# Performance work log

Measured on AMD Instinct MI355X. Metric: run time of the kernel, lower is better.

## Reference

```python
import jax, jax.numpy as jnp
import numpy as np

N = 100000     # total points
PBS = 500      # point_batch_size (hard-coded in module)
K = 100        # num_neighbors
KP = 15        # num_kernel_points
EPS = 1e-5


def _bn(x, g, b, axes):
    # torch BatchNorm in training mode: batch stats, biased variance
    m = jnp.mean(x, axis=axes, keepdims=True)
    v = jnp.var(x, axis=axes, keepdims=True)
    return (x - m) / jnp.sqrt(v + EPS) * g + b


def setup_inputs() -> dict:
    key = jax.random.key(0)
    ks = jax.random.split(key, 16)
    rn = lambda k, sh, s=1.0: jax.random.normal(k, sh, jnp.float32) * s
    return {
        "pts": rn(ks[0], (N, 3)),
        "normal": rn(ks[1], (N, 3)),
        "kp_points": rn(ks[2], (KP, 3)),
        "kp_weights": rn(ks[3], (KP, 3, 128), 0.3),
        "kp_sigma": jnp.float32(1.0),
        "conv1_w": rn(ks[4], (1024, 128), 128 ** -0.5),
        "conv1_b": rn(ks[5], (1024,), 0.02),
        "bn1_g": jnp.ones((1024,), jnp.float32),
        "bn1_b": jnp.zeros((1024,), jnp.float32),
        "fc1_w": rn(ks[6], (512, 1024), 1024 ** -0.5),
        "fc1_b": rn(ks[7], (512,), 0.02),
        "bn4_g": jnp.ones((512,), jnp.float32),
        "bn4_b": jnp.zeros((512,), jnp.float32),
        "fc2_w": rn(ks[8], (256, 512), 512 ** -0.5),
        "fc2_b": rn(ks[9], (256,), 0.02),
        "bn5_g": jnp.ones((256,), jnp.float32),
        "bn5_b": jnp.zeros((256,), jnp.float32),
        "fc3_w": rn(ks[10], (3, 256), 256 ** -0.5),
        "fc3_b": rn(ks[11], (3,), 0.02),
        "index": jax.random.randint(ks[12], (PBS,), 0, N, jnp.int32),
    }


def reference(pts, normal, kp_points, kp_weights, kp_sigma,
              conv1_w, conv1_b, bn1_g, bn1_b,
              fc1_w, fc1_b, bn4_g, bn4_b,
              fc2_w, fc2_b, bn5_g, bn5_b,
              fc3_w, fc3_b, index):
    sel = pts[index]                                               # [B,3]
    # L-inf pairwise distance and kNN (topk of -dist, as in the torch code)
    dist = jnp.max(jnp.abs(sel[:, None, :] - pts[None, :, :]), axis=-1)  # [B,N]
    _, nbr = jax.lax.top_k(-dist, K)                               # [B,K]
    rel = pts[nbr] - sel[:, None, :]                               # [B,K,3]

    # KPConv: gaussian weights vs kernel points, per-kernel-point linear map
    d2 = jnp.sum((rel[:, :, None, :] - kp_points[None, None]) ** 2, axis=-1)  # [B,K,KP]
    w = jnp.exp(-0.5 * d2 / (kp_sigma ** 2))
    wf = rel[:, :, None, :] * w[..., None]                         # [B,K,KP,3]
    h = jax.nn.relu(jnp.einsum('bnkc,kco->bno', wf, kp_weights))   # [B,K,128]

    # 1x1 conv 128->1024, relu then BN over (batch, points) per channel
    h = jnp.einsum('bnc,oc->bno', h, conv1_w) + conv1_b            # [B,K,1024]
    h = _bn(jax.nn.relu(h), bn1_g, bn1_b, (0, 1))
    feat = jnp.max(h, axis=1)                                      # [B,1024]

    feat = _bn(jax.nn.relu(feat @ fc1_w.T + fc1_b), bn4_g, bn4_b, (0,))
    feat = _bn(jax.nn.relu(feat @ fc2_w.T + fc2_b), bn5_g, bn5_b, (0,))
    feat = feat @ fc3_w.T + fc3_b                                  # [B,3]
    return feat, normal[index]
```

## Files before the change

kernel.cpp:

```cpp
#include <hip/hip_runtime.h>
#include <hip/hip_fp16.h>

#define NPTS 100000
#define NB 500
#define KNN 100
#define KPN 15
#define C1 128
#define C2 1024
#define C3 512
#define C4 256

#define G 64
#define NCELLS (G * G * G)
#define GB 5.0f
#define GINVH ((float)G / (2.f * GB))
#define CAND_CAP 2048

typedef _Float16 half8 __attribute__((ext_vector_type(8)));
typedef float f32x4 __attribute__((ext_vector_type(4)));

__global__ __launch_bounds__(256) void prep_kernel(
    const float* __restrict__ pts, const float* __restrict__ normal,
    const int* __restrict__ index, const float* __restrict__ w1,
    const float* __restrict__ kpw, float* __restrict__ sel,
    float* __restrict__ out2, __half* __restrict__ wh,
    __half* __restrict__ kpwT_hi, __half* __restrict__ kpwT_lo) {
  int i = blockIdx.x * 256 + threadIdx.x;
  if (i < NB) {
    int ix = index[i];
    sel[i * 3 + 0] = pts[3 * ix + 0];
    sel[i * 3 + 1] = pts[3 * ix + 1];
    sel[i * 3 + 2] = pts[3 * ix + 2];
    out2[i * 3 + 0] = normal[3 * ix + 0];
    out2[i * 3 + 1] = normal[3 * ix + 1];
    out2[i * 3 + 2] = normal[3 * ix + 2];
  }
  if (i < C2 * C1) wh[i] = __float2half(w1[i]);
  if (i < 128 * 64) {
    int o = i >> 6, j = i & 63;
    float v = (j < 45) ? kpw[j * 128 + o] : 0.f;
    __half hi = __float2half_rn(v);
    kpwT_hi[i] = hi;
    kpwT_lo[i] = __float2half_rn(v - __half2float(hi));
  }
}

__device__ __forceinline__ int cell_coord(float x) {
  int c = (int)floorf((x + GB) * GINVH);
  return min(max(c, 0), G - 1);
}
__device__ __forceinline__ int cell_of(float x, float y, float z) {
  return (cell_coord(x) << 12) | (cell_coord(y) << 6) | cell_coord(z);
}

__global__ __launch_bounds__(256) void grid_hist_kernel(
    const float* __restrict__ pts, unsigned* __restrict__ cnt) {
  int i = blockIdx.x * 256 + threadIdx.x;
  if (i >= NPTS) return;
  atomicAdd(&cnt[cell_of(pts[3 * i], pts[3 * i + 1], pts[3 * i + 2])], 1u);
}

__global__ __launch_bounds__(256) void grid_scan1_kernel(
    const unsigned* __restrict__ cnt, unsigned* __restrict__ cursor,
    unsigned* __restrict__ chunktot) {
  const int tid = threadIdx.x;
  int base = blockIdx.x * 1024 + tid * 4;
  unsigned c0 = cnt[base], c1 = cnt[base + 1], c2 = cnt[base + 2],
           c3 = cnt[base + 3];
  unsigned tot = c0 + c1 + c2 + c3;
  __shared__ unsigned sb[256];
  sb[tid] = tot;
  __syncthreads();
  for (int off = 1; off < 256; off <<= 1) {
    unsigned add = (tid >= off) ? sb[tid - off] : 0u;
    __syncthreads();
    sb[tid] += add;
    __syncthreads();
  }
  unsigned excl = sb[tid] - tot;
  cursor[base] = excl;
  cursor[base + 1] = excl + c0;
  cursor[base + 2] = excl + c0 + c1;
  cursor[base + 3] = excl + c0 + c1 + c2;
  if (tid == 255) chunktot[blockIdx.x] = sb[255];
}

__global__ __launch_bounds__(256) void grid_scan2_kernel(
    const unsigned* __restrict__ chunktot, unsigned* __restrict__ chunkoff) {
  const int tid = threadIdx.x;
  unsigned v = chunktot[tid];
  __shared__ unsigned sb[256];
  sb[tid] = v;
  __syncthreads();
  for (int off = 1; off < 256; off <<= 1) {
    unsigned add = (tid >= off) ? sb[tid - off] : 0u;
    __syncthreads();
    sb[tid] += add;
    __syncthreads();
  }
  chunkoff[tid] = sb[tid] - v;
}

__global__ __launch_bounds__(256) void grid_scan3_kernel(
    unsigned* __restrict__ cursor, const unsigned* __restrict__ chunkoff) {
  unsigned off = chunkoff[blockIdx.x];
  int base = blockIdx.x * 1024 + threadIdx.x * 4;
#pragma unroll
  for (int j = 0; j < 4; ++j) cursor[base + j] += off;
}

__global__ __launch_bounds__(256) void grid_scatter_kernel(
    const float* __restrict__ pts, unsigned* __restrict__ cursor,
    float4* __restrict__ sorted) {
  int i = blockIdx.x * 256 + threadIdx.x;
  if (i >= NPTS) return;
  float x = pts[3 * i], y = pts[3 * i + 1], z = pts[3 * i + 2];
  unsigned pos = atomicAdd(&cursor[cell_of(x, y, z)], 1u);
  sorted[pos] = make_float4(x, y, z, __int_as_float(i));
}

__device__ __forceinline__ unsigned linf_bits(float px, float py, float pz,
                                              float sx, float sy, float sz) {
  float dx = fabsf(px - sx), dy = fabsf(py - sy), dz = fabsf(pz - sz);
  return __float_as_uint(fmaxf(fmaxf(dx, dy), dz));
}

__global__ __launch_bounds__(256) void knn_kernel(
    const float4* __restrict__ sorted, const unsigned* __restrict__ cnt,
    const unsigned* __restrict__ cursor,
    const float* __restrict__ sel, int* __restrict__ nbr) {
  const int b = blockIdx.x;
  const int tid = threadIdx.x;
  __shared__ unsigned cbits[CAND_CAP];
  __shared__ int cidx[CAND_CAP];
  __shared__ unsigned hist[4096];
  __shared__ unsigned scanbuf[256];
  __shared__ int s_total, s_m, s_mc, s_chunk;
  __shared__ unsigned s_excl, s_bub;

  const float qx = sel[b * 3 + 0], qy = sel[b * 3 + 1], qz = sel[b * 3 + 2];
  const int qcx = cell_coord(qx), qcy = cell_coord(qy), qcz = cell_coord(qz);

  int s = 0;
  int xlo, xhi, ylo, yhi, zlo, zhi;
  for (;;) {
    if (tid == 0) s_total = 0;
    __syncthreads();
    xlo = max(qcx - s, 0); xhi = min(qcx + s, G - 1);
    ylo = max(qcy - s, 0); yhi = min(qcy + s, G - 1);
    zlo = max(qcz - s, 0); zhi = min(qcz + s, G - 1);
    int nx = xhi - xlo + 1, ny = yhi - ylo + 1, nz = zhi - zlo + 1;
    int ncell = nx * ny * nz;
    unsigned local = 0;
    for (int ci = tid; ci < ncell; ci += 256) {
      int cz = ci % nz;
      int r = ci / nz;
      int cy = r % ny;
      int cx = r / ny;
      local += cnt[((xlo + cx) << 12) | ((ylo + cy) << 6) | (zlo + cz)];
    }
#pragma unroll
    for (int off = 32; off; off >>= 1) local += __shfl_down(local, off);
    if ((tid & 63) == 0) atomicAdd(&s_total, (int)local);
    __syncthreads();
    if (s_total >= KNN || (xlo == 0 && ylo == 0 && zlo == 0 && xhi == G - 1 &&
                           yhi == G - 1 && zhi == G - 1))
      break;
    ++s;
    __syncthreads();
  }

  if (tid == 0) s_m = 0;
  __syncthreads();
  {
    int nx = xhi - xlo + 1, ny = yhi - ylo + 1, nz = zhi - zlo + 1;
    int ncell = nx * ny * nz;
    for (int ci = tid; ci < ncell; ci += 256) {
      int cz = ci % nz;
      int r = ci / nz;
      int cy = r % ny;
      int cx = r / ny;
      int cell = ((xlo + cx) << 12) | ((ylo + cy) << 6) | (zlo + cz);
      unsigned end = cursor[cell];
      unsigned beg = end - cnt[cell];
      for (unsigned p = beg; p < end; ++p) {
        float4 f = sorted[p];
        unsigned bits = linf_bits(f.x, f.y, f.z, qx, qy, qz);
        int e = atomicAdd(&s_m, 1);
        if (e < CAND_CAP) {
          cbits[e] = bits;
          cidx[e] = __float_as_int(f.w);
        }
      }
    }
  }
  __syncthreads();
  int m = s_m < CAND_CAP ? s_m : CAND_CAP;

  for (int j = tid; j < 4096; j += 256) hist[j] = 0;
  __syncthreads();
  for (int e = tid; e < m; e += 256) atomicAdd(&hist[cbits[e] >> 19], 1u);
  __syncthreads();
  unsigned csum = 0;
  {
    int c0 = tid * 16;
#pragma unroll
    for (int j = 0; j < 16; ++j) csum += hist[c0 + j];
  }
  scanbuf[tid] = csum;
  __syncthreads();
  for (int off = 1; off < 256; off <<= 1) {
    unsigned add = (tid >= off) ? scanbuf[tid - off] : 0u;
    __syncthreads();
    scanbuf[tid] += add;
    __syncthreads();
  }
  {
    unsigned incl = scanbuf[tid], excl = incl - csum;
    if (excl < KNN && KNN <= incl) {
      s_chunk = tid;
      s_excl = excl;
    }
  }
  __syncthreads();
  if (tid == 0) {
    unsigned cum = s_excl;
    int bin = s_chunk * 16;
    while (cum + hist[bin] < KNN) {
      cum += hist[bin];
      ++bin;
    }
    s_bub = (unsigned)(bin + 1) << 19;
  }
  __syncthreads();

  const unsigned bub = s_bub;
  const float dub = __uint_as_float(bub);
  if (tid == 0) s_mc = 0;
  __syncthreads();
  {
    int xlo2 = min(max((int)floorf((qx - dub + GB) * GINVH), 0), G - 1);
    int xhi2 = min(max((int)floorf((qx + dub + GB) * GINVH), 0), G - 1);
    int ylo2 = min(max((int)floorf((qy - dub + GB) * GINVH), 0), G - 1);
    int yhi2 = min(max((int)floorf((qy + dub + GB) * GINVH), 0), G - 1);
    int zlo2 = min(max((int)floorf((qz - dub + GB) * GINVH), 0), G - 1);
    int zhi2 = min(max((int)floorf((qz + dub + GB) * GINVH), 0), G - 1);
    int nx = xhi2 - xlo2 + 1, ny = yhi2 - ylo2 + 1, nz = zhi2 - zlo2 + 1;
    int ncell = nx * ny * nz;
    for (int ci = tid; ci < ncell; ci += 256) {
      int cz = ci % nz;
      int r = ci / nz;
      int cy = r % ny;
      int cx = r / ny;
      int cell = ((xlo2 + cx) << 12) | ((ylo2 + cy) << 6) | (zlo2 + cz);
      unsigned end = cursor[cell];
      unsigned beg = end - cnt[cell];
      for (unsigned p = beg; p < end; ++p) {
        float4 f = sorted[p];
        unsigned bits = linf_bits(f.x, f.y, f.z, qx, qy, qz);
        if (bits < bub) {
          int e = atomicAdd(&s_mc, 1);
          if (e < CAND_CAP) {
            cbits[e] = bits;
            cidx[e] = __float_as_int(f.w);
          }
        }
      }
    }
  }
  __syncthreads();
  int mc = s_mc < CAND_CAP ? s_mc : CAND_CAP;

  for (int c = tid; c < mc; c += 256) {
    unsigned bc = cbits[c];
    int ic = cidx[c];
    int rank = 0;
    for (int j = 0; j < mc; ++j) {
      unsigned bj = cbits[j];
      rank += (bj < bc || (bj == bc && cidx[j] < ic)) ? 1 : 0;
    }
    if (rank < KNN) nbr[b * KNN + rank] = ic;
  }
}

__global__ __launch_bounds__(256) void kpconv_mfma_kernel(
    const float* __restrict__ pts, const float* __restrict__ sel,
    const int* __restrict__ nbr, const float* __restrict__ kp_points,
    const __half* __restrict__ kpwT_hi, const __half* __restrict__ kpwT_lo,
    const float* __restrict__ kp_sigma, __half* __restrict__ h) {
  const int b = blockIdx.x;
  const int tid = threadIdx.x;
  const int wave = tid >> 6, lane = tid & 63;
  const int lr = lane & 15, quad = lane >> 4;
  __shared__ __half As_hi[112 * 72];
  __shared__ __half As_lo[112 * 72];
  __shared__ __half Bs_hi[128 * 72];
  __shared__ __half Bs_lo[128 * 72];
  __shared__ float rel[100][4];
  __shared__ float kpp[48];

  for (int i = tid; i < 128 * 8; i += 256) {
    int row = i >> 3, seg = i & 7;
    *(float4*)&Bs_hi[row * 72 + seg * 8] =
        *(const float4*)&kpwT_hi[row * 64 + seg * 8];
    *(float4*)&Bs_lo[row * 72 + seg * 8] =
        *(const float4*)&kpwT_lo[row * 64 + seg * 8];
  }
  {
    float4 z = make_float4(0.f, 0.f, 0.f, 0.f);
    for (int i = tid; i < 112 * 8; i += 256) {
      int row = i >> 3, seg = i & 7;
      *(float4*)&As_hi[row * 72 + seg * 8] = z;
      *(float4*)&As_lo[row * 72 + seg * 8] = z;
    }
  }
  if (tid < 45) kpp[tid] = kp_points[tid];
  if (tid < 100) {
    int idx = nbr[b * KNN + tid];
    rel[tid][0] = pts[3 * idx + 0] - sel[b * 3 + 0];
    rel[tid][1] = pts[3 * idx + 1] - sel[b * 3 + 1];
    rel[tid][2] = pts[3 * idx + 2] - sel[b * 3 + 2];
  }
  __syncthreads();

  const float sg = kp_sigma[0];
  const float inv2s2 = -0.5f / (sg * sg);
  for (int i = tid; i < 100 * KPN; i += 256) {
    int k = i / KPN, p = i - k * KPN;
    float rx = rel[k][0] - kpp[p * 3 + 0];
    float ry = rel[k][1] - kpp[p * 3 + 1];
    float rz = rel[k][2] - kpp[p * 3 + 2];
    float w = expf(inv2s2 * (rx * rx + ry * ry + rz * rz));
#pragma unroll
    for (int c = 0; c < 3; ++c) {
      float a = rel[k][c] * w;
      __half hi = __float2half_rn(a);
      As_hi[k * 72 + p * 3 + c] = hi;
      As_lo[k * 72 + p * 3 + c] = __float2half_rn(a - __half2float(hi));
    }
  }
  __syncthreads();

  f32x4 acc[2][7];
#pragma unroll
  for (int t = 0; t < 2; ++t)
#pragma unroll
    for (int m = 0; m < 7; ++m) acc[t][m] = (f32x4)(0.f);

#pragma unroll
  for (int s = 0; s < 2; ++s) {
    half8 bhi[2], blo[2];
#pragma unroll
    for (int t = 0; t < 2; ++t) {
      int boff = ((wave * 2 + t) * 16 + lr) * 72 + s * 32 + quad * 8;
      bhi[t] = *(const half8*)&Bs_hi[boff];
      blo[t] = *(const half8*)&Bs_lo[boff];
    }
#pragma unroll
    for (int m = 0; m < 7; ++m) {
      int aoff = (m * 16 + lr) * 72 + s * 32 + quad * 8;
      half8 ahi = *(const half8*)&As_hi[aoff];
      half8 alo = *(const half8*)&As_lo[aoff];
#pragma unroll
      for (int t = 0; t < 2; ++t) {
        acc[t][m] = __builtin_amdgcn_mfma_f32_16x16x32_f16(ahi, bhi[t],
                                                           acc[t][m], 0, 0, 0);
        acc[t][m] = __builtin_amdgcn_mfma_f32_16x16x32_f16(ahi, blo[t],
                                                           acc[t][m], 0, 0, 0);
        acc[t][m] = __builtin_amdgcn_mfma_f32_16x16x32_f16(alo, bhi[t],
                                                           acc[t][m], 0, 0, 0);
      }
    }
  }

#pragma unroll
  for (int t = 0; t < 2; ++t) {
    int col = (wave * 2 + t) * 16 + lr;
#pragma unroll
    for (int m = 0; m < 7; ++m)
#pragma unroll
      for (int r = 0; r < 4; ++r) {
        int row = m * 16 + quad * 4 + r;
        if (row < 100)
          h[(b * KNN + row) * 128 + col] =
              __float2half_rn(fmaxf(acc[t][m][r], 0.f));
      }
  }
}

__global__ __launch_bounds__(256) void conv1_mfma_kernel(
    const __half* __restrict__ h16, const __half* __restrict__ wh,
    const float* __restrict__ bias, float* __restrict__ featmax,
    float* __restrict__ featmin, float* __restrict__ bnsum,
    float* __restrict__ bnsq) {
  const int b = blockIdx.y;
  const int n0 = blockIdx.x * 128;
  const int tid = threadIdx.x;
  const int wave = tid >> 6, lane = tid & 63;
  const int lr = lane & 15, quad = lane >> 4;
  __shared__ __half Hs[112 * 136];
  __shared__ __half Ws[128 * 136];

  for (int i = tid; i < 112 * 16; i += 256) {
    int row = i >> 4, seg = i & 15;
    float4 v = make_float4(0.f, 0.f, 0.f, 0.f);
    if (row < 100) v = *(const float4*)&h16[(b * 100 + row) * 128 + seg * 8];
    *(float4*)&Hs[row * 136 + seg * 8] = v;
  }
  for (int i = tid; i < 128 * 16; i += 256) {
    int row = i >> 4, seg = i & 15;
    *(float4*)&Ws[row * 136 + seg * 8] =
        *(const float4*)&wh[(n0 + row) * 128 + seg * 8];
  }
  __syncthreads();

  f32x4 acc[2][7];
#pragma unroll
  for (int t = 0; t < 2; ++t)
#pragma unroll
    for (int m = 0; m < 7; ++m) acc[t][m] = (f32x4)(0.f);

#pragma unroll
  for (int s = 0; s < 4; ++s) {
    half8 bfrag[2];
#pragma unroll
    for (int t = 0; t < 2; ++t)
      bfrag[t] =
          *(const half8*)&Ws[((wave * 2 + t) * 16 + lr) * 136 + s * 32 + quad * 8];
#pragma unroll
    for (int m = 0; m < 7; ++m) {
      half8 afrag = *(const half8*)&Hs[(m * 16 + lr) * 136 + s * 32 + quad * 8];
      acc[0][m] =
          __builtin_amdgcn_mfma_f32_16x16x32_f16(afrag, bfrag[0], acc[0][m], 0, 0, 0);
      acc[1][m] =
          __builtin_amdgcn_mfma_f32_16x16x32_f16(afrag, bfrag[1], acc[1][m], 0, 0, 0);
    }
  }

#pragma unroll
  for (int t = 0; t < 2; ++t) {
    int col = n0 + (wave * 2 + t) * 16 + lr;
    float bv = bias[col];
    float pmax = -1e30f, pmin = 1e30f, psum = 0.f, psq = 0.f;
#pragma unroll
    for (int m = 0; m < 7; ++m)
#pragma unroll
      for (int r = 0; r < 4; ++r) {
        int row = m * 16 + quad * 4 + r;
        if (row < 100) {
          float y = fmaxf(acc[t][m][r] + bv, 0.f);
          pmax = fmaxf(pmax, y);
          pmin = fminf(pmin, y);
          psum += y;
          psq += y * y;
        }
      }
    pmax = fmaxf(pmax, __shfl_xor(pmax, 16));
    pmax = fmaxf(pmax, __shfl_xor(pmax, 32));
    pmin = fminf(pmin, __shfl_xor(pmin, 16));
    pmin = fminf(pmin, __shfl_xor(pmin, 32));
    psum += __shfl_xor(psum, 16);
    psum += __shfl_xor(psum, 32);
    psq += __shfl_xor(psq, 16);
    psq += __shfl_xor(psq, 32);
    if (quad == 0) {
      featmax[b * C2 + col] = pmax;
      featmin[b * C2 + col] = pmin;
      atomicAdd(&bnsum[col], psum);
      atomicAdd(&bnsq[col], psq);
    }
  }
}

__global__ __launch_bounds__(256) void bn1max_kernel(
    const float* __restrict__ featmax, const float* __restrict__ featmin,
    const float* __restrict__ bnsum, const float* __restrict__ bnsq,
    const float* __restrict__ g, const float* __restrict__ bb,
    float* __restrict__ feat1) {
  int idx = blockIdx.x * 256 + threadIdx.x;
  if (idx >= NB * C2) return;
  int o = idx & (C2 - 1);
  const float invn = 1.f / (float)(NB * KNN);
  float m = bnsum[o] * invn;
  float v = bnsq[o] * invn - m * m;
  float a = g[o] / sqrtf(v + 1e-5f);
  float x = (a >= 0.f) ? featmax[idx] : featmin[idx];
  feat1[idx] = (x - m) * a + bb[o];
}

template <int KDIM>
__global__ __launch_bounds__(256) void fc_relu_stats_kernel(
    const float* __restrict__ x,
    const float* __restrict__ w,
    const float* __restrict__ bias, float* __restrict__ yraw,
    float* __restrict__ s, float* __restrict__ sq, int ncols) {
  const int r0 = blockIdx.x * 4;
  const int n0 = blockIdx.y * 64;
  const int tid = threadIdx.x;
  const int col = tid >> 2;
  const int row = tid & 3;
  __shared__ float xs[4][1028];
  __shared__ float ws[64][132];
  for (int f = tid; f < KDIM; f += 256) {
    int rr = f / (KDIM / 4), kq = (f % (KDIM / 4)) * 4;
    *(float4*)&xs[rr][kq] = *(const float4*)&x[(r0 + rr) * KDIM + kq];
  }
  float acc = 0.f;
  for (int kc = 0; kc < KDIM; kc += 128) {
    __syncthreads();
#pragma unroll
    for (int i = 0; i < 8; ++i) {
      int f = tid + i * 256;
      int cr = f >> 5, kq = (f & 31) * 4;
      *(float4*)&ws[cr][kq] = *(const float4*)&w[(n0 + cr) * KDIM + kc + kq];
    }
    __syncthreads();
    for (int kk = 0; kk < 128; kk += 4) {
      float4 xv = *(float4*)&xs[row][kc + kk];
      float4 wv = *(float4*)&ws[col][kk];
      acc += xv.x * wv.x + xv.y * wv.y + xv.z * wv.z + xv.w * wv.w;
    }
  }
  float y = fmaxf(acc + bias[n0 + col], 0.f);
  yraw[(r0 + row) * ncols + n0 + col] = y;
  float ys = y, y2 = y * y;
  ys += __shfl_xor(ys, 1); y2 += __shfl_xor(y2, 1);
  ys += __shfl_xor(ys, 2); y2 += __shfl_xor(y2, 2);
  if (row == 0) {
    atomicAdd(&s[n0 + col], ys);
    atomicAdd(&sq[n0 + col], y2);
  }
}

__global__ __launch_bounds__(256) void bn_finalize_kernel(
    const float* __restrict__ yraw, const float* __restrict__ s,
    const float* __restrict__ sq, const float* __restrict__ g,
    const float* __restrict__ bb, float* __restrict__ out, int ncols) {
  int idx = blockIdx.x * 256 + threadIdx.x;
  if (idx >= NB * ncols) return;
  int o = idx & (ncols - 1);
  float m = s[o] * (1.f / (float)NB);
  float v = sq[o] * (1.f / (float)NB) - m * m;
  float a = g[o] / sqrtf(v + 1e-5f);
  out[idx] = (yraw[idx] - m) * a + bb[o];
}

__global__ __launch_bounds__(256) void fc3_kernel(
    const float* __restrict__ feat, const float* __restrict__ w,
    const float* __restrict__ bias, float* __restrict__ out) {
  int idx = blockIdx.x * 256 + threadIdx.x;
  if (idx >= NB * 3) return;
  int b = idx / 3, o = idx % 3;
  float acc = 0.f;
  for (int k = 0; k < C4; ++k) acc += feat[b * C4 + k] * w[o * C4 + k];
  out[idx] = acc + bias[o];
}

extern "C" void kernel_launch(void* const* d_in, const int* in_sizes, int n_in,
                              void* d_out, int out_size, void* d_ws,
                              size_t ws_size, hipStream_t stream) {
  const float* pts = (const float*)d_in[0];
  const float* normal = (const float*)d_in[1];
  const float* kp_points = (const float*)d_in[2];
  const float* kp_weights = (const float*)d_in[3];
  const float* kp_sigma = (const float*)d_in[4];
  const float* conv1_w = (const float*)d_in[5];
  const float* conv1_b = (const float*)d_in[6];
  const float* bn1_g = (const float*)d_in[7];
  const float* bn1_b = (const float*)d_in[8];
  const float* fc1_w = (const float*)d_in[9];
  const float* fc1_b = (const float*)d_in[10];
  const float* bn4_g = (const float*)d_in[11];
  const float* bn4_b = (const float*)d_in[12];
  const float* fc2_w = (const float*)d_in[13];
  const float* fc2_b = (const float*)d_in[14];
  const float* bn5_g = (const float*)d_in[15];
  const float* bn5_b = (const float*)d_in[16];
  const float* fc3_w = (const float*)d_in[17];
  const float* fc3_b = (const float*)d_in[18];
  const int* index = (const int*)d_in[19];
  float* out = (float*)d_out;

  char* p = (char*)d_ws;
  auto carve = [&](size_t bytes) {
    void* r = (void*)p;
    p += (bytes + 255) & ~(size_t)255;
    return r;
  };
  float* sel = (float*)carve(NB * 3 * 4);
  int* nbr = (int*)carve(NB * KNN * 4);
  __half* h = (__half*)carve((size_t)NB * KNN * C1 * 2);
  __half* wh = (__half*)carve((size_t)C2 * C1 * 2);
  __half* kpwT_hi = (__half*)carve((size_t)128 * 64 * 2);
  __half* kpwT_lo = (__half*)carve((size_t)128 * 64 * 2);
  float* featmax = (float*)carve(NB * C2 * 4);
  float* featmin = (float*)carve(NB * C2 * 4);
  float* feat1 = (float*)carve(NB * C2 * 4);
  float* f2raw = (float*)carve(NB * C3 * 4);
  float* feat2 = (float*)carve(NB * C3 * 4);
  float* f3raw = (float*)carve(NB * C4 * 4);
  float* feat3 = (float*)carve(NB * C4 * 4);
  float* stats = (float*)carve((2 * C2 + 2 * C3 + 2 * C4) * 4);
  float* bnsum = stats;
  float* bnsq = stats + C2;
  float* s4 = stats + 2 * C2;
  float* sq4 = s4 + C3;
  float* s5 = sq4 + C3;
  float* sq5 = s5 + C4;

  {
    char* gp = (char*)h;
    auto gcarve = [&](size_t bytes) {
      void* r = (void*)gp;
      gp += (bytes + 255) & ~(size_t)255;
      return r;
    };
    unsigned* cellcnt = (unsigned*)gcarve((size_t)NCELLS * 4);
    unsigned* cellcur = (unsigned*)gcarve((size_t)NCELLS * 4);
    unsigned* chunktot = (unsigned*)gcarve(256 * 4);
    unsigned* chunkoff = (unsigned*)gcarve(256 * 4);
    float4* sortedpts = (float4*)gcarve((size_t)NPTS * 16);

    hipMemsetAsync(stats, 0, (2 * C2 + 2 * C3 + 2 * C4) * 4, stream);
    hipMemsetAsync(cellcnt, 0, (size_t)NCELLS * 4, stream);

    prep_kernel<<<(C2 * C1 + 255) / 256, 256, 0, stream>>>(
        pts, normal, index, conv1_w, kp_weights, sel, out + NB * 3, wh,
        kpwT_hi, kpwT_lo);
    grid_hist_kernel<<<(NPTS + 255) / 256, 256, 0, stream>>>(pts, cellcnt);
    grid_scan1_kernel<<<256, 256, 0, stream>>>(cellcnt, cellcur, chunktot);
    grid_scan2_kernel<<<1, 256, 0, stream>>>(chunktot, chunkoff);
    grid_scan3_kernel<<<256, 256, 0, stream>>>(cellcur, chunkoff);
    grid_scatter_kernel<<<(NPTS + 255) / 256, 256, 0, stream>>>(pts, cellcur,
                                                                sortedpts);
    knn_kernel<<<NB, 256, 0, stream>>>(sortedpts, cellcnt, cellcur, sel, nbr);
  }

  kpconv_mfma_kernel<<<NB, 256, 0, stream>>>(pts, sel, nbr, kp_points, kpwT_hi,
                                             kpwT_lo, kp_sigma, h);
  conv1_mfma_kernel<<<dim3(8, NB), 256, 0, stream>>>(h, wh, conv1_b, featmax,
                                                     featmin, bnsum, bnsq);
  bn1max_kernel<<<(NB * C2 + 255) / 256, 256, 0, stream>>>(
      featmax, featmin, bnsum, bnsq, bn1_g, bn1_b, feat1);
  fc_relu_stats_kernel<C2><<<dim3(125, C3 / 64), 256, 0, stream>>>(
      feat1, fc1_w, fc1_b, f2raw, s4, sq4, C3);
  bn_finalize_kernel<<<(NB * C3 + 255) / 256, 256, 0, stream>>>(
      f2raw, s4, sq4, bn4_g, bn4_b, feat2, C3);
  fc_relu_stats_kernel<C3><<<dim3(125, C4 / 64), 256, 0, stream>>>(
      feat2, fc2_w, fc2_b, f3raw, s5, sq5, C4);
  bn_finalize_kernel<<<(NB * C4 + 255) / 256, 256, 0, stream>>>(
      f3raw, s5, sq5, bn5_g, bn5_b, feat3, C4);
  fc3_kernel<<<(NB * 3 + 255) / 256, 256, 0, stream>>>(feat3, fc3_w, fc3_b,
                                                       out);
}
```

Before: 298.1 us.

## Fuse KPConv and conv1 into one kernel keeping features in shared memory

Merges the KPConv MFMA kernel and the 128->1024 conv1 MFMA kernel into one per-batch-point kernel. The KPConv output is written to shared memory instead of a global fp16 buffer, and the block then loops over eight 128-column chunks of the conv1 weights, reusing the same shared tile. This removes the global write and read of the intermediate features and one launch. In exchange the grid shrinks from 4000 blocks to 500, each doing serial work. The larger shared memory footprint (~71KB) may also cut occupancy.

```diff
diff --git a/kernel.cpp b/kernel.cpp
--- a/kernel.cpp
+++ b/kernel.cpp
@@ -283,21 +283,28 @@
   }
 }
 
-__global__ __launch_bounds__(256) void kpconv_mfma_kernel(
+__global__ __launch_bounds__(256) void kpconv_conv1_kernel(
     const float* __restrict__ pts, const float* __restrict__ sel,
     const int* __restrict__ nbr, const float* __restrict__ kp_points,
     const __half* __restrict__ kpwT_hi, const __half* __restrict__ kpwT_lo,
-    const float* __restrict__ kp_sigma, __half* __restrict__ h) {
+    const float* __restrict__ kp_sigma, const __half* __restrict__ wh,
+    const float* __restrict__ bias, float* __restrict__ featmax,
+    float* __restrict__ featmin, float* __restrict__ bnsum,
+    float* __restrict__ bnsq) {
   const int b = blockIdx.x;
   const int tid = threadIdx.x;
   const int wave = tid >> 6, lane = tid & 63;
   const int lr = lane & 15, quad = lane >> 4;
-  __shared__ __half As_hi[112 * 72];
-  __shared__ __half As_lo[112 * 72];
-  __shared__ __half Bs_hi[128 * 72];
-  __shared__ __half Bs_lo[128 * 72];
-  __shared__ float rel[100][4];
-  __shared__ float kpp[48];
+
+  __shared__ __align__(16) char smem[71168];
+  __half* As_hi = (__half*)smem;
+  __half* As_lo = As_hi + 112 * 72;
+  __half* Bs_hi = As_lo + 112 * 72;
+  __half* Bs_lo = Bs_hi + 128 * 72;
+  float* rel = (float*)(Bs_lo + 128 * 72);
+  float* kpp = rel + 100 * 4;
+  __half* Hs = (__half*)smem;
+  __half* Ws = Hs + 112 * 136;
 
   for (int i = tid; i < 128 * 8; i += 256) {
     int row = i >> 3, seg = i & 7;
@@ -317,9 +324,9 @@
   if (tid < 45) kpp[tid] = kp_points[tid];
   if (tid < 100) {
     int idx = nbr[b * KNN + tid];
-    rel[tid][0] = pts[3 * idx + 0] - sel[b * 3 + 0];
-    rel[tid][1] = pts[3 * idx + 1] - sel[b * 3 + 1];
-    rel[tid][2] = pts[3 * idx + 2] - sel[b * 3 + 2];
+    rel[tid * 4 + 0] = pts[3 * idx + 0] - sel[b * 3 + 0];
+    rel[tid * 4 + 1] = pts[3 * idx + 1] - sel[b * 3 + 1];
+    rel[tid * 4 + 2] = pts[3 * idx + 2] - sel[b * 3 + 2];
   }
   __syncthreads();
 
@@ -327,13 +334,13 @@
   const float inv2s2 = -0.5f / (sg * sg);
   for (int i = tid; i < 100 * KPN; i += 256) {
     int k = i / KPN, p = i - k * KPN;
-    float rx = rel[k][0] - kpp[p * 3 + 0];
-    float ry = rel[k][1] - kpp[p * 3 + 1];
-    float rz = rel[k][2] - kpp[p * 3 + 2];
+    float rx = rel[k * 4 + 0] - kpp[p * 3 + 0];
+    float ry = rel[k * 4 + 1] - kpp[p * 3 + 1];
+    float rz = rel[k * 4 + 2] - kpp[p * 3 + 2];
     float w = expf(inv2s2 * (rx * rx + ry * ry + rz * rz));
 #pragma unroll
     for (int c = 0; c < 3; ++c) {
-      float a = rel[k][c] * w;
+      float a = rel[k * 4 + c] * w;
       __half hi = __float2half_rn(a);
       As_hi[k * 72 + p * 3 + c] = hi;
       As_lo[k * 72 + p * 3 + c] = __float2half_rn(a - __half2float(hi));
@@ -372,6 +379,7 @@
       }
     }
   }
+  __syncthreads();
 
 #pragma unroll
   for (int t = 0; t < 2; ++t) {
@@ -381,93 +389,75 @@
 #pragma unroll
       for (int r = 0; r < 4; ++r) {
         int row = m * 16 + quad * 4 + r;
-        if (row < 100)
-          h[(b * KNN + row) * 128 + col] =
-              __float2half_rn(fmaxf(acc[t][m][r], 0.f));
+        Hs[row * 136 + col] = __float2half_rn(fmaxf(acc[t][m][r], 0.f));
       }
   }
-}
-
-__global__ __launch_bounds__(256) void conv1_mfma_kernel(
-    const __half* __restrict__ h16, const __half* __restrict__ wh,
-    const float* __restrict__ bias, float* __restrict__ featmax,
-    float* __restrict__ featmin, float* __restrict__ bnsum,
-    float* __restrict__ bnsq) {
-  const int b = blockIdx.y;
-  const int n0 = blockIdx.x * 128;
-  const int tid = threadIdx.x;
-  const int wave = tid >> 6, lane = tid & 63;
-  const int lr = lane & 15, quad = lane >> 4;
-  __shared__ __half Hs[112 * 136];
-  __shared__ __half Ws[128 * 136];
-
-  for (int i = tid; i < 112 * 16; i += 256) {
-    int row = i >> 4, seg = i & 15;
-    float4 v = make_float4(0.f, 0.f, 0.f, 0.f);
-    if (row < 100) v = *(const float4*)&h16[(b * 100 + row) * 128 + seg * 8];
-    *(float4*)&Hs[row * 136 + seg * 8] = v;
-  }
-  for (int i = tid; i < 128 * 16; i += 256) {
-    int row = i >> 4, seg = i & 15;
-    *(float4*)&Ws[row * 136 + seg * 8] =
-        *(const float4*)&wh[(n0 + row) * 128 + seg * 8];
-  }
-  __syncthreads();
-
-  f32x4 acc[2][7];
-#pragma unroll
-  for (int t = 0; t < 2; ++t)
-#pragma unroll
-    for (int m = 0; m < 7; ++m) acc[t][m] = (f32x4)(0.f);
-
-#pragma unroll
-  for (int s = 0; s < 4; ++s) {
-    half8 bfrag[2];
+
+  for (int c = 0; c < 8; ++c) {
+    __syncthreads();
+    for (int i = tid; i < 128 * 16; i += 256) {
+      int row = i >> 4, seg = i & 15;
+      *(float4*)&Ws[row * 136 + seg * 8] =
+          *(const float4*)&wh[(c * 128 + row) * 128 + seg * 8];
+    }
+    __syncthreads();
+
+    f32x4 acc2[2][7];
 #pragma unroll
     for (int t = 0; t < 2; ++t)
-      bfrag[t] =
-          *(const half8*)&Ws[((wave * 2 + t) * 16 + lr) * 136 + s * 32 + quad * 8];
-#pragma unroll
-    for (int m = 0; m < 7; ++m) {
-      half8 afrag = *(const half8*)&Hs[(m * 16 + lr) * 136 + s * 32 + quad * 8];
-      acc[0][m] =
-          __builtin_amdgcn_mfma_f32_16x16x32_f16(afrag, bfrag[0], acc[0][m], 0, 0, 0);
-      acc[1][m] =
-          __builtin_amdgcn_mfma_f32_16x16x32_f16(afrag, bfrag[1], acc[1][m], 0, 0, 0);
-    }
-  }
-
-#pragma unroll
-  for (int t = 0; t < 2; ++t) {
-    int col = n0 + (wave * 2 + t) * 16 + lr;
-    float bv = bias[col];
-    float pmax = -1e30f, pmin = 1e30f, psum = 0.f, psq = 0.f;
-#pragma unroll
-    for (int m = 0; m < 7; ++m)
-#pragma unroll
-      for (int r = 0; r < 4; ++r) {
-        int row = m * 16 + quad * 4 + r;
-        if (row < 100) {
-          float y = fmaxf(acc[t][m][r] + bv, 0.f);
-          pmax = fmaxf(pmax, y);
-          pmin = fminf(pmin, y);
-          psum += y;
-          psq += y * y;
+#pragma unroll
+      for (int m = 0; m < 7; ++m) acc2[t][m] = (f32x4)(0.f);
+
+#pragma unroll
+    for (int s = 0; s < 4; ++s) {
+      half8 bfrag[2];
+#pragma unroll
+      for (int t = 0; t < 2; ++t)
+        bfrag[t] = *(const half8*)&Ws[((wave * 2 + t) * 16 + lr) * 136 +
+                                      s * 32 + quad * 8];
+#pragma unroll
+      for (int m = 0; m < 7; ++m) {
+        half8 afrag =
+            *(const half8*)&Hs[(m * 16 + lr) * 136 + s * 32 + quad * 8];
+        acc2[0][m] = __builtin_amdgcn_mfma_f32_16x16x32_f16(afrag, bfrag[0],
+                                                            acc2[0][m], 0, 0, 0);
+        acc2[1][m] = __builtin_amdgcn_mfma_f32_16x16x32_f16(afrag, bfrag[1],
+                                                            acc2[1][m], 0, 0, 0);
+      }
+    }
+
+#pragma unroll
+    for (int t = 0; t < 2; ++t) {
+      int col = c * 128 + (wave * 2 + t) * 16 + lr;
+      float bv = bias[col];
+      float pmax = -1e30f, pmin = 1e30f, psum = 0.f, psq = 0.f;
+#pragma unroll
+      for (int m = 0; m < 7; ++m)
+#pragma unroll
+        for (int r = 0; r < 4; ++r) {
+          int row = m * 16 + quad * 4 + r;
+          if (row < 100) {
+            float y = fmaxf(acc2[t][m][r] + bv, 0.f);
+            pmax = fmaxf(pmax, y);
+            pmin = fminf(pmin, y);
+            psum += y;
+            psq += y * y;
+          }
         }
+      pmax = fmaxf(pmax, __shfl_xor(pmax, 16));
+      pmax = fmaxf(pmax, __shfl_xor(pmax, 32));
+      pmin = fminf(pmin, __shfl_xor(pmin, 16));
+      pmin = fminf(pmin, __shfl_xor(pmin, 32));
+      psum += __shfl_xor(psum, 16);
+      psum += __shfl_xor(psum, 32);
+      psq += __shfl_xor(psq, 16);
+      psq += __shfl_xor(psq, 32);
+      if (quad == 0) {
+        featmax[b * C2 + col] = pmax;
+        featmin[b * C2 + col] = pmin;
+        atomicAdd(&bnsum[col], psum);
+        atomicAdd(&bnsq[col], psq);
       }
-    pmax = fmaxf(pmax, __shfl_xor(pmax, 16));
-    pmax = fmaxf(pmax, __shfl_xor(pmax, 32));
-    pmin = fminf(pmin, __shfl_xor(pmin, 16));
-    pmin = fminf(pmin, __shfl_xor(pmin, 32));
-    psum += __shfl_xor(psum, 16);
-    psum += __shfl_xor(psum, 32);
-    psq += __shfl_xor(psq, 16);
-    psq += __shfl_xor(psq, 32);
-    if (quad == 0) {
-      featmax[b * C2 + col] = pmax;
-      featmin[b * C2 + col] = pmin;
-      atomicAdd(&bnsum[col], psum);
-      atomicAdd(&bnsq[col], psq);
     }
   }
 }
@@ -589,7 +579,6 @@
   };
   float* sel = (float*)carve(NB * 3 * 4);
   int* nbr = (int*)carve(NB * KNN * 4);
-  __half* h = (__half*)carve((size_t)NB * KNN * C1 * 2);
   __half* wh = (__half*)carve((size_t)C2 * C1 * 2);
   __half* kpwT_hi = (__half*)carve((size_t)128 * 64 * 2);
   __half* kpwT_lo = (__half*)carve((size_t)128 * 64 * 2);
@@ -607,39 +596,28 @@
   float* sq4 = s4 + C3;
   float* s5 = sq4 + C3;
   float* sq5 = s5 + C4;
-
-  {
-    char* gp = (char*)h;
-    auto gcarve = [&](size_t bytes) {
-      void* r = (void*)gp;
-      gp += (bytes + 255) & ~(size_t)255;
-      return r;
-    };
-    unsigned* cellcnt = (unsigned*)gcarve((size_t)NCELLS * 4);
-    unsigned* cellcur = (unsigned*)gcarve((size_t)NCELLS * 4);
-    unsigned* chunktot = (unsigned*)gcarve(256 * 4);
-    unsigned* chunkoff = (unsigned*)gcarve(256 * 4);
-    float4* sortedpts = (float4*)gcarve((size_t)NPTS * 16);
-
-    hipMemsetAsync(stats, 0, (2 * C2 + 2 * C3 + 2 * C4) * 4, stream);
-    hipMemsetAsync(cellcnt, 0, (size_t)NCELLS * 4, stream);
-
-    prep_kernel<<<(C2 * C1 + 255) / 256, 256, 0, stream>>>(
-        pts, normal, index, conv1_w, kp_weights, sel, out + NB * 3, wh,
-        kpwT_hi, kpwT_lo);
-    grid_hist_kernel<<<(NPTS + 255) / 256, 256, 0, stream>>>(pts, cellcnt);
-    grid_scan1_kernel<<<256, 256, 0, stream>>>(cellcnt, cellcur, chunktot);
-    grid_scan2_kernel<<<1, 256, 0, stream>>>(chunktot, chunkoff);
-    grid_scan3_kernel<<<256, 256, 0, stream>>>(cellcur, chunkoff);
-    grid_scatter_kernel<<<(NPTS + 255) / 256, 256, 0, stream>>>(pts, cellcur,
-                                                                sortedpts);
-    knn_kernel<<<NB, 256, 0, stream>>>(sortedpts, cellcnt, cellcur, sel, nbr);
-  }
-
-  kpconv_mfma_kernel<<<NB, 256, 0, stream>>>(pts, sel, nbr, kp_points, kpwT_hi,
-                                             kpwT_lo, kp_sigma, h);
-  conv1_mfma_kernel<<<dim3(8, NB), 256, 0, stream>>>(h, wh, conv1_b, featmax,
-                                                     featmin, bnsum, bnsq);
+  unsigned* cellcnt = (unsigned*)carve((size_t)NCELLS * 4);
+  unsigned* cellcur = (unsigned*)carve((size_t)NCELLS * 4);
+  unsigned* chunktot = (unsigned*)carve(256 * 4);
+  unsigned* chunkoff = (unsigned*)carve(256 * 4);
+  float4* sortedpts = (float4*)carve((size_t)NPTS * 16);
+
+  hipMemsetAsync(stats, 0, (2 * C2 + 2 * C3 + 2 * C4) * 4, stream);
+  hipMemsetAsync(cellcnt, 0, (size_t)NCELLS * 4, stream);
+
+  prep_kernel<<<(C2 * C1 + 255) / 256, 256, 0, stream>>>(
+      pts, normal, index, conv1_w, kp_weights, sel, out + NB * 3, wh, kpwT_hi,
+      kpwT_lo);
+  grid_hist_kernel<<<(NPTS + 255) / 256, 256, 0, stream>>>(pts, cellcnt);
+  grid_scan1_kernel<<<256, 256, 0, stream>>>(cellcnt, cellcur, chunktot);
+  grid_scan2_kernel<<<1, 256, 0, stream>>>(chunktot, chunkoff);
+  grid_scan3_kernel<<<256, 256, 0, stream>>>(cellcur, chunkoff);
+  grid_scatter_kernel<<<(NPTS + 255) / 256, 256, 0, stream>>>(pts, cellcur,
+                                                              sortedpts);
+  knn_kernel<<<NB, 256, 0, stream>>>(sortedpts, cellcnt, cellcur, sel, nbr);
+  kpconv_conv1_kernel<<<NB, 256, 0, stream>>>(
+      pts, sel, nbr, kp_points, kpwT_hi, kpwT_lo, kp_sigma, wh, conv1_b,
+      featmax, featmin, bnsum, bnsq);
   bn1max_kernel<<<(NB * C2 + 255) / 256, 256, 0, stream>>>(
       featmax, featmin, bnsum, bnsq, bn1_g, bn1_b, feat1);
   fc_relu_stats_kernel<C2><<<dim3(125, C3 / 64), 256, 0, stream>>>(
```

New measurement: 285.1 us. 1.05x faster.
